# Kernel optimization log

Hardware: AMD Instinct MI355X
Metric: run time of the kernel (lower is better)

## Reference

```python
import jax, jax.numpy as jnp
import numpy as np

B, N, S = 8, 4096, 1024
D1, D2 = 128, 256
IN_CH, OUT_CH = D1 + D2, 256
BN_EPS = 1e-5


def setup_inputs() -> dict:
    key = jax.random.key(0)
    ks = jax.random.split(key, 12)
    inp = {
        "xyz1": jax.random.normal(ks[0], (B, N, 3), jnp.float32),
        "xyz2": jax.random.normal(ks[1], (B, S, 3), jnp.float32),
        "points1": jax.random.normal(ks[2], (B, N, D1), jnp.float32),
        "points2": jax.random.normal(ks[3], (B, S, D2), jnp.float32),
        # fuse: Conv1d(in_ch->out_ch, k=1) + BN
        "W_fuse": jax.random.normal(ks[4], (OUT_CH, IN_CH), jnp.float32) * (1.0 / np.sqrt(IN_CH)),
        "b_fuse": jnp.zeros((OUT_CH,), jnp.float32),
        "g_fuse": jnp.ones((OUT_CH,), jnp.float32),
        "bt_fuse": jnp.zeros((OUT_CH,), jnp.float32),
        # res block net1: Conv1d(out_ch->out_ch) + BN (res_expansion=1.0)
        "W1": jax.random.normal(ks[5], (OUT_CH, OUT_CH), jnp.float32) * (1.0 / np.sqrt(OUT_CH)),
        "b1": jnp.zeros((OUT_CH,), jnp.float32),
        "g1": jnp.ones((OUT_CH,), jnp.float32),
        "bt1": jnp.zeros((OUT_CH,), jnp.float32),
        # res block net2: Conv1d(out_ch->out_ch) + BN
        "W2": jax.random.normal(ks[6], (OUT_CH, OUT_CH), jnp.float32) * (1.0 / np.sqrt(OUT_CH)),
        "b2": jnp.zeros((OUT_CH,), jnp.float32),
        "g2": jnp.ones((OUT_CH,), jnp.float32),
        "bt2": jnp.zeros((OUT_CH,), jnp.float32),
    }
    return inp


def _bn(x, g, b):
    # BatchNorm1d training-mode forward: stats over (batch, length), x: [B, C, L]
    m = jnp.mean(x, axis=(0, 2), keepdims=True)
    v = jnp.var(x, axis=(0, 2), keepdims=True)
    return (x - m) * jax.lax.rsqrt(v + BN_EPS) * g[None, :, None] + b[None, :, None]


def _conv1x1(x, W, b):
    # x: [B, C_in, L], W: [C_out, C_in] -> [B, C_out, L]
    return jnp.einsum("oc,bcl->bol", W, x) + b[None, :, None]


def _gelu(x):
    return jax.nn.gelu(x, approximate=False)  # torch nn.GELU default (erf)


def reference(xyz1, xyz2, points1, points2,
              W_fuse, b_fuse, g_fuse, bt_fuse,
              W1, b1, g1, bt1, W2, b2, g2, bt2):
    # squared pairwise distances [B, N, S] without B x N x S x 3 intermediate
    d = (jnp.sum(xyz1 * xyz1, -1)[:, :, None]
         - 2.0 * jnp.einsum("bnc,bsc->bns", xyz1, xyz2)
         + jnp.sum(xyz2 * xyz2, -1)[:, None, :])
    # 3 nearest coarse points per dense point (== sort ascending, take first 3)
    neg_d3, idx = jax.lax.top_k(-d, 3)            # [B, N, 3]
    d3 = -neg_d3
    recip = 1.0 / (d3 + 1e-8)
    w = recip / jnp.sum(recip, axis=2, keepdims=True)  # [B, N, 3]
    gathered = points2[jnp.arange(points2.shape[0])[:, None, None], idx]  # [B, N, 3, D2]
    interp = jnp.sum(gathered * w[..., None], axis=2)  # [B, N, D2]

    new_points = jnp.concatenate([points1, interp], axis=-1)  # [B, N, D1+D2]
    x = jnp.transpose(new_points, (0, 2, 1))                   # [B, C, N]

    # fuse: conv-bn-gelu
    x = _gelu(_bn(_conv1x1(x, W_fuse, b_fuse), g_fuse, bt_fuse))
    # residual block: gelu(bn(conv(gelu(bn(conv(x))))) + x)
    y = _gelu(_bn(_conv1x1(x, W1, b1), g1, bt1))
    y = _bn(_conv1x1(y, W2, b2), g2, bt2)
    x = _gelu(y + x)

    return jnp.transpose(x, (0, 2, 1))  # [B, N, out_ch]
```

## Files before the change

### kernel.cpp

```cpp
#include <hip/hip_runtime.h>
#include <hip/hip_bf16.h>

constexpr int Bb = 8, Nn = 4096, Ss = 1024;
constexpr int D1 = 128, D2 = 256, KIN = 384, OC = 256;
constexpr int L = Bb * Nn;
constexpr float BN_EPS = 1e-5f;

typedef __attribute__((ext_vector_type(4))) float floatx4;
typedef __attribute__((ext_vector_type(8))) __bf16 bf16x8;

#define DEV __device__ __forceinline__

DEV float bf2f(unsigned short u) {
    union { unsigned int i; float f; } v; v.i = ((unsigned int)u) << 16; return v.f;
}
DEV unsigned short f2bf(float f) {
    union { float f; unsigned int i; } v; v.f = f;
    unsigned int x = v.i;
    return (unsigned short)((x + 0x7FFFu + ((x >> 16) & 1u)) >> 16);
}
DEV float gelu_f(float x) {
    float u = x * (0.7978845608f + 0.0356774081f * x * x);
    float t = __expf(-2.0f * u);
    return x * __builtin_amdgcn_rcpf(1.0f + t);
}

DEV bool probe_isf(const unsigned int* __restrict__ w, int tid) {
    unsigned int lo = w[tid & 63] & 0xFFFFu;
    int e = (int)((lo >> 7) & 0xFF);
    unsigned long long m = __ballot(e >= 100 && e <= 144);
    return __popcll(m) < 48;
}

template <int K> DEV int permoff(int off) {
    int row = off / K, rr = off - row * K;
    int cg_ = (rr >> 3) & 7;
    return row * K + (rr & ~63) + (((cg_ ^ (row & 7)) << 3)) + (rr & 7);
}

DEV void merge3(float& d0, float& d1, float& d2, int& i0, int& i1, int& i2,
                float e0, float e1, float e2, int j0, int j1, int j2, bool pref) {
    float a0 = d0, a1 = d1, a2 = d2; int x0 = i0, x1 = i1, x2 = i2;
    float b0 = e0, b1 = e1;          int y0 = j0, y1 = j1;
    bool t = pref ? (a0 <= b0) : (a0 < b0);
    d0 = t ? a0 : b0; i0 = t ? x0 : y0;
    a0 = t ? a1 : a0; x0 = t ? x1 : x0;
    a1 = t ? a2 : a1; x1 = t ? x2 : x1;
    b0 = t ? b0 : b1; y0 = t ? y0 : y1;
    b1 = t ? b1 : e2; y1 = t ? y1 : j2;
    t = pref ? (a0 <= b0) : (a0 < b0);
    d1 = t ? a0 : b0; i1 = t ? x0 : y0;
    a0 = t ? a1 : a0; x0 = t ? x1 : x0;
    b0 = t ? b0 : b1; y0 = t ? y0 : y1;
    t = pref ? (a0 <= b0) : (a0 < b0);
    d2 = t ? a0 : b0; i2 = t ? x0 : y0;
}

__global__ __launch_bounds__(256) void k_front(const void* __restrict__ xyz1_,
                                               const void* __restrict__ xyz2_,
                                               const void* __restrict__ w0_,
                                               const void* __restrict__ w1_,
                                               const void* __restrict__ w2_,
                                               unsigned short* __restrict__ Wdst,
                                               float* __restrict__ stats,
                                               int* __restrict__ dflag,
                                               int* __restrict__ nn_idx,
                                               float* __restrict__ nn_w) {
    int tid = threadIdx.x;
    int bid = blockIdx.x;
    bool isf = probe_isf((const unsigned int*)xyz1_, tid);

    if (bid < 6) {
        stats[bid * 256 + tid] = 0.0f;
        if (bid == 0 && tid == 0) *dflag = isf ? 1 : 0;
        return;
    }
    if (bid < 902) {
        int i = (bid - 6) * 256 + tid;
        const void* src; int off;
        if (i < 98304)       { src = w0_; off = permoff<384>(i); }
        else if (i < 163840) { src = w1_; off = permoff<256>(i - 98304); }
        else                 { src = w2_; off = permoff<256>(i - 163840); }
        Wdst[i] = isf ? f2bf(((const float*)src)[off]) : ((const unsigned short*)src)[off];
        return;
    }

    __shared__ alignas(16) float s4[Ss * 4 + 32];
    int bn0 = (bid - 902) * 32;
    int b = bn0 >> 12;

    if (isf) {
        const float* p2 = (const float*)xyz2_ + (size_t)b * Ss * 3;
        for (int i = tid; i < Ss * 3; i += 256) {
            int s = i / 3, k = i - s * 3;
            s4[s * 4 + k + ((s >> 7) << 2)] = p2[i];
        }
    } else {
        const unsigned short* p2 = (const unsigned short*)xyz2_ + (size_t)b * Ss * 3;
        for (int i = tid; i < Ss * 3; i += 256) {
            int s = i / 3, k = i - s * 3;
            s4[s * 4 + k + ((s >> 7) << 2)] = bf2f(p2[i]);
        }
    }
    __syncthreads();
    for (int s = tid; s < Ss; s += 256) {
        int a = s * 4 + ((s >> 7) << 2);
        float x = s4[a], y = s4[a + 1], z = s4[a + 2];
        s4[a + 3] = x * x + y * y + z * z;
    }
    __syncthreads();

    int part = tid & 7;
    int bn = bn0 + (tid >> 3);
    float x1, y1, z1;
    if (isf) {
        const float* p1 = (const float*)xyz1_ + (size_t)bn * 3;
        x1 = p1[0]; y1 = p1[1]; z1 = p1[2];
    } else {
        const unsigned short* p1 = (const unsigned short*)xyz1_ + (size_t)bn * 3;
        x1 = bf2f(p1[0]); y1 = bf2f(p1[1]); z1 = bf2f(p1[2]);
    }
    float n1 = x1 * x1 + y1 * y1 + z1 * z1;

    float d0 = 3.4e38f, d1 = 3.4e38f, d2 = 3.4e38f;
    int i0 = 0, i1 = 0, i2 = 0;
    const float* sp = &s4[part * 516];
#pragma unroll 4
    for (int j = 0; j < 128; ++j) {
        float4 qv = *(const float4*)(sp + j * 4);
        float d = n1 + qv.w - 2.0f * (x1 * qv.x + y1 * qv.y + z1 * qv.z);
        int s = part * 128 + j;
        bool c2 = d < d2, c1 = d < d1, c0 = d < d0;
        d2 = c1 ? d1 : (c2 ? d : d2); i2 = c1 ? i1 : (c2 ? s : i2);
        d1 = c0 ? d0 : (c1 ? d : d1); i1 = c0 ? i0 : (c1 ? s : i1);
        d0 = c0 ? d  : d0;            i0 = c0 ? s  : i0;
    }
#pragma unroll
    for (int m = 1; m <= 4; m <<= 1) {
        float e0 = __shfl_xor(d0, m, 64), e1 = __shfl_xor(d1, m, 64), e2 = __shfl_xor(d2, m, 64);
        int   j0 = __shfl_xor(i0, m, 64), j1 = __shfl_xor(i1, m, 64), j2 = __shfl_xor(i2, m, 64);
        bool pref = (part < (part ^ m));
        merge3(d0, d1, d2, i0, i1, i2, e0, e1, e2, j0, j1, j2, pref);
    }
    if (part == 0) {
        float r0 = 1.0f / (d0 + 1e-8f), r1 = 1.0f / (d1 + 1e-8f), r2 = 1.0f / (d2 + 1e-8f);
        float rs = 1.0f / (r0 + r1 + r2);
        nn_idx[bn * 3 + 0] = i0; nn_idx[bn * 3 + 1] = i1; nn_idx[bn * 3 + 2] = i2;
        nn_w[bn * 3 + 0] = r0 * rs; nn_w[bn * 3 + 1] = r1 * rs; nn_w[bn * 3 + 2] = r2 * rs;
    }
}

__global__ __launch_bounds__(256, 4) void k_gemm1(const void* __restrict__ p1_,
                                                  const void* __restrict__ p2_,
                                                  const int* __restrict__ nn_idx,
                                                  const float* __restrict__ nn_w,
                                                  const int* __restrict__ dflag,
                                                  const unsigned short* __restrict__ W,
                                                  unsigned short* __restrict__ Out,
                                                  float* __restrict__ S1, float* __restrict__ S2) {
    __shared__ alignas(16) unsigned short As[32 * 64];
    __shared__ alignas(16) unsigned short Bs[256 * 64];
    __shared__ float sS1[256], sS2[256];

    int tid = threadIdx.x;
    int l0 = blockIdx.x * 32;
    int wn = tid >> 6, lane = tid & 63, quad = lane >> 4, lr = lane & 15;
    bool isf = (*dflag != 0);

    floatx4 acc[2][4];
#pragma unroll
    for (int mi = 0; mi < 2; ++mi)
#pragma unroll
        for (int ni = 0; ni < 4; ++ni) acc[mi][ni] = (floatx4){0.f, 0.f, 0.f, 0.f};

    for (int kc = 0; kc < KIN / 64; ++kc) {
        __syncthreads();
#pragma unroll
        for (int it = 0; it < 8; ++it) {
            int chunk = it * 4 + wn;
            int row = chunk * 8 + (lane >> 3);
            int cg_ = lane & 7;
            const unsigned short* src = W + (size_t)row * KIN + kc * 64 + cg_ * 8;
            __builtin_amdgcn_global_load_lds(
                (const __attribute__((address_space(1))) void*)src,
                (__attribute__((address_space(3))) void*)&Bs[chunk * 512],
                16, 0, 0);
        }
        {
            int row = tid >> 3, c8 = tid & 7;
            int pt = l0 + row;
            int c0 = kc * 64 + c8 * 8;
            union { uint4 v; unsigned short u[8]; } va;
            if (c0 < D1) {
                if (isf) {
                    const float* p = (const float*)p1_ + (size_t)pt * D1 + c0;
                    float4 f0 = *(const float4*)p;
                    float4 f1 = *(const float4*)(p + 4);
                    va.u[0] = f2bf(f0.x); va.u[1] = f2bf(f0.y); va.u[2] = f2bf(f0.z); va.u[3] = f2bf(f0.w);
                    va.u[4] = f2bf(f1.x); va.u[5] = f2bf(f1.y); va.u[6] = f2bf(f1.z); va.u[7] = f2bf(f1.w);
                } else {
                    va.v = *(const uint4*)((const unsigned short*)p1_ + (size_t)pt * D1 + c0);
                }
            } else {
                int c2 = c0 - D1;
                int b = pt >> 12;
                int j0 = nn_idx[pt * 3], j1 = nn_idx[pt * 3 + 1], j2 = nn_idx[pt * 3 + 2];
                float w0 = nn_w[pt * 3], w1 = nn_w[pt * 3 + 1], w2 = nn_w[pt * 3 + 2];
                if (isf) {
                    const float* base = (const float*)p2_;
                    const float* r0 = base + ((size_t)(b * Ss + j0)) * D2 + c2;
                    const float* r1 = base + ((size_t)(b * Ss + j1)) * D2 + c2;
                    const float* r2 = base + ((size_t)(b * Ss + j2)) * D2 + c2;
#pragma unroll
                    for (int h = 0; h < 2; ++h) {
                        float4 a0 = *(const float4*)(r0 + h * 4);
                        float4 a1 = *(const float4*)(r1 + h * 4);
                        float4 a2 = *(const float4*)(r2 + h * 4);
                        va.u[h * 4 + 0] = f2bf(w0 * a0.x + w1 * a1.x + w2 * a2.x);
                        va.u[h * 4 + 1] = f2bf(w0 * a0.y + w1 * a1.y + w2 * a2.y);
                        va.u[h * 4 + 2] = f2bf(w0 * a0.z + w1 * a1.z + w2 * a2.z);
                        va.u[h * 4 + 3] = f2bf(w0 * a0.w + w1 * a1.w + w2 * a2.w);
                    }
                } else {
                    const unsigned short* base = (const unsigned short*)p2_;
                    uint4 v0 = *(const uint4*)(base + ((size_t)(b * Ss + j0)) * D2 + c2);
                    uint4 v1 = *(const uint4*)(base + ((size_t)(b * Ss + j1)) * D2 + c2);
                    uint4 v2 = *(const uint4*)(base + ((size_t)(b * Ss + j2)) * D2 + c2);
                    const unsigned short* u0 = (const unsigned short*)&v0;
                    const unsigned short* u1 = (const unsigned short*)&v1;
                    const unsigned short* u2 = (const unsigned short*)&v2;
#pragma unroll
                    for (int j = 0; j < 8; ++j)
                        va.u[j] = f2bf(w0 * bf2f(u0[j]) + w1 * bf2f(u1[j]) + w2 * bf2f(u2[j]));
                }
            }
            *(uint4*)&As[row * 64 + ((c8 ^ (row & 7)) << 3)] = va.v;
        }
        __syncthreads();
#pragma unroll
        for (int ks8 = 0; ks8 < 2; ++ks8) {
            bf16x8 af[2], bfr[4];
#pragma unroll
            for (int mi = 0; mi < 2; ++mi) {
                int ra = mi * 16 + lr;
                af[mi] = *(const bf16x8*)&As[ra * 64 + ((((ks8 << 2) + quad) ^ (ra & 7)) << 3)];
            }
#pragma unroll
            for (int ni = 0; ni < 4; ++ni) {
                int rb = wn * 64 + ni * 16 + lr;
                bfr[ni] = *(const bf16x8*)&Bs[rb * 64 + ((((ks8 << 2) + quad) ^ (rb & 7)) << 3)];
            }
#pragma unroll
            for (int mi = 0; mi < 2; ++mi)
#pragma unroll
                for (int ni = 0; ni < 4; ++ni)
                    acc[mi][ni] = __builtin_amdgcn_mfma_f32_16x16x32_bf16(af[mi], bfr[ni], acc[mi][ni], 0, 0, 0);
        }
    }

    float p1a[4] = {0, 0, 0, 0}, p2a[4] = {0, 0, 0, 0};
#pragma unroll
    for (int mi = 0; mi < 2; ++mi)
#pragma unroll
        for (int ni = 0; ni < 4; ++ni)
#pragma unroll
            for (int r = 0; r < 4; ++r) {
                float v = acc[mi][ni][r];
                int row = l0 + mi * 16 + quad * 4 + r;
                int col = wn * 64 + ni * 16 + lr;
                Out[(size_t)row * OC + col] = f2bf(v);
                p1a[ni] += v; p2a[ni] += v * v;
            }
    sS1[tid] = 0.f; sS2[tid] = 0.f;
    __syncthreads();
#pragma unroll
    for (int ni = 0; ni < 4; ++ni) {
        atomicAdd(&sS1[wn * 64 + ni * 16 + lr], p1a[ni]);
        atomicAdd(&sS2[wn * 64 + ni * 16 + lr], p2a[ni]);
    }
    __syncthreads();
    atomicAdd(&S1[tid], sS1[tid]);
    atomicAdd(&S2[tid], sS2[tid]);
}

__global__ __launch_bounds__(256, 4) void k_gemm(const unsigned short* __restrict__ A,
                                                 const unsigned short* __restrict__ W,
                                                 unsigned short* __restrict__ Out,
                                                 float* __restrict__ S1, float* __restrict__ S2,
                                                 const float* __restrict__ S1in,
                                                 const float* __restrict__ S2in,
                                                 const void* __restrict__ g_,
                                                 const void* __restrict__ bt_,
                                                 const int* __restrict__ dflag) {
    __shared__ alignas(16) unsigned short As[64 * 64];
    __shared__ alignas(16) unsigned short Bs[128 * 64];
    __shared__ float sS1[128], sS2[128];
    __shared__ float sCA[256], sCC[256];

    int tid = threadIdx.x;
    int l0 = (blockIdx.x >> 1) * 64;
    int n0 = (blockIdx.x & 1) * 128;
    int wn = tid >> 6, lane = tid & 63, quad = lane >> 4, lr = lane & 15;
    int wr = wn >> 1, wc = wn & 1;

    {
        float m = S1in[tid] * (1.0f / (float)L);
        float var = S2in[tid] * (1.0f / (float)L) - m * m;
        float g, bt;
        if (*dflag) { g = ((const float*)g_)[tid]; bt = ((const float*)bt_)[tid]; }
        else { g = bf2f(((const unsigned short*)g_)[tid]); bt = bf2f(((const unsigned short*)bt_)[tid]); }
        float a = g * rsqrtf(var + BN_EPS);
        sCA[tid] = a;
        sCC[tid] = bt - m * a;
        if (tid < 128) { sS1[tid] = 0.f; sS2[tid] = 0.f; }
    }

    floatx4 acc[2][4];
#pragma unroll
    for (int mi = 0; mi < 2; ++mi)
#pragma unroll
        for (int ni = 0; ni < 4; ++ni) acc[mi][ni] = (floatx4){0.f, 0.f, 0.f, 0.f};

    for (int kc = 0; kc < OC / 64; ++kc) {
        __syncthreads();
#pragma unroll
        for (int it = 0; it < 4; ++it) {
            int chunk = it * 4 + wn;
            int row = chunk * 8 + (lane >> 3);
            int cg_ = lane & 7;
            const unsigned short* src = W + (size_t)(n0 + row) * OC + kc * 64 + cg_ * 8;
            __builtin_amdgcn_global_load_lds(
                (const __attribute__((address_space(1))) void*)src,
                (__attribute__((address_space(3))) void*)&Bs[chunk * 512],
                16, 0, 0);
        }
#pragma unroll
        for (int it = 0; it < 2; ++it) {
            int idx = it * 256 + tid, row = idx >> 3, c8 = idx & 7;
            union { uint4 v; unsigned short u[8]; } va;
            va.v = *(const uint4*)(A + (size_t)(l0 + row) * OC + kc * 64 + c8 * 8);
            int kb = kc * 64 + c8 * 8;
#pragma unroll
            for (int j = 0; j < 8; ++j) {
                float f = bf2f(va.u[j]);
                va.u[j] = f2bf(gelu_f(sCA[kb + j] * f + sCC[kb + j]));
            }
            *(uint4*)&As[row * 64 + ((c8 ^ (row & 7)) << 3)] = va.v;
        }
        __syncthreads();
#pragma unroll
        for (int ks8 = 0; ks8 < 2; ++ks8) {
            bf16x8 af[2], bfr[4];
#pragma unroll
            for (int mi = 0; mi < 2; ++mi) {
                int ra = wr * 32 + mi * 16 + lr;
                af[mi] = *(const bf16x8*)&As[ra * 64 + ((((ks8 << 2) + quad) ^ (ra & 7)) << 3)];
            }
#pragma unroll
            for (int ni = 0; ni < 4; ++ni) {
                int rb = wc * 64 + ni * 16 + lr;
                bfr[ni] = *(const bf16x8*)&Bs[rb * 64 + ((((ks8 << 2) + quad) ^ (rb & 7)) << 3)];
            }
#pragma unroll
            for (int mi = 0; mi < 2; ++mi)
#pragma unroll
                for (int ni = 0; ni < 4; ++ni)
                    acc[mi][ni] = __builtin_amdgcn_mfma_f32_16x16x32_bf16(af[mi], bfr[ni], acc[mi][ni], 0, 0, 0);
        }
    }

    float p1a[4] = {0, 0, 0, 0}, p2a[4] = {0, 0, 0, 0};
#pragma unroll
    for (int mi = 0; mi < 2; ++mi)
#pragma unroll
        for (int ni = 0; ni < 4; ++ni)
#pragma unroll
            for (int r = 0; r < 4; ++r) {
                float v = acc[mi][ni][r];
                int row = l0 + wr * 32 + mi * 16 + quad * 4 + r;
                int col = n0 + wc * 64 + ni * 16 + lr;
                Out[(size_t)row * OC + col] = f2bf(v);
                p1a[ni] += v; p2a[ni] += v * v;
            }
    __syncthreads();
#pragma unroll
    for (int ni = 0; ni < 4; ++ni) {
        atomicAdd(&sS1[wc * 64 + ni * 16 + lr], p1a[ni]);
        atomicAdd(&sS2[wc * 64 + ni * 16 + lr], p2a[ni]);
    }
    __syncthreads();
    if (tid < 128) {
        atomicAdd(&S1[n0 + tid], sS1[tid]);
        atomicAdd(&S2[n0 + tid], sS2[tid]);
    }
}

__global__ __launch_bounds__(256) void k_final(const unsigned short* __restrict__ t0,
                                               const unsigned short* __restrict__ t2,
                                               const float* __restrict__ S1_0, const float* __restrict__ S2_0,
                                               const float* __restrict__ S1_2, const float* __restrict__ S2_2,
                                               const void* __restrict__ g0_, const void* __restrict__ bt0_,
                                               const void* __restrict__ g2_, const void* __restrict__ bt2_,
                                               const int* __restrict__ dflag,
                                               void* __restrict__ out_) {
    __shared__ float sA0[256], sC0[256], sA2[256], sC2[256];
    int tid = threadIdx.x;
    bool isf = (*dflag != 0);
    {
        float m0 = S1_0[tid] * (1.0f / (float)L);
        float v0_ = S2_0[tid] * (1.0f / (float)L) - m0 * m0;
        float m2 = S1_2[tid] * (1.0f / (float)L);
        float v2_ = S2_2[tid] * (1.0f / (float)L) - m2 * m2;
        float g0, b0, g2, b2;
        if (isf) {
            g0 = ((const float*)g0_)[tid]; b0 = ((const float*)bt0_)[tid];
            g2 = ((const float*)g2_)[tid]; b2 = ((const float*)bt2_)[tid];
        } else {
            g0 = bf2f(((const unsigned short*)g0_)[tid]); b0 = bf2f(((const unsigned short*)bt0_)[tid]);
            g2 = bf2f(((const unsigned short*)g2_)[tid]); b2 = bf2f(((const unsigned short*)bt2_)[tid]);
        }
        float a0 = g0 * rsqrtf(v0_ + BN_EPS);
        float a2 = g2 * rsqrtf(v2_ + BN_EPS);
        sA0[tid] = a0; sC0[tid] = b0 - m0 * a0;
        sA2[tid] = a2; sC2[tid] = b2 - m2 * a2;
    }
    __syncthreads();

    int idx = (blockIdx.x * 256 + tid) * 8;
    int col = idx & (OC - 1);
    union { uint4 v; unsigned short u[8]; } v0, v2;
    v0.v = *(const uint4*)(t0 + idx);
    v2.v = *(const uint4*)(t2 + idx);
    float r[8];
#pragma unroll
    for (int j = 0; j < 8; ++j) {
        float x = gelu_f(sA0[col + j] * bf2f(v0.u[j]) + sC0[col + j]);
        float y = sA2[col + j] * bf2f(v2.u[j]) + sC2[col + j];
        r[j] = gelu_f(x + y);
    }
    if (isf) {
        float* o = (float*)out_ + idx;
        float4 lo = {r[0], r[1], r[2], r[3]};
        float4 hi = {r[4], r[5], r[6], r[7]};
        *(float4*)o = lo;
        *(float4*)(o + 4) = hi;
    } else {
        union { uint4 v; unsigned short u[8]; } vo;
#pragma unroll
        for (int j = 0; j < 8; ++j) vo.u[j] = f2bf(r[j]);
        *(uint4*)((unsigned short*)out_ + idx) = vo.v;
    }
}

extern "C" void kernel_launch(void* const* d_in, const int* in_sizes, int n_in,
                              void* d_out, int out_size, void* d_ws, size_t ws_size,
                              hipStream_t stream) {
    const void* xyz1    = d_in[0];
    const void* xyz2    = d_in[1];
    const void* points1 = d_in[2];
    const void* points2 = d_in[3];
    const void* W_fuse  = d_in[4];
    const void* g_fuse  = d_in[6];
    const void* bt_fuse = d_in[7];
    const void* W1      = d_in[8];
    const void* g1      = d_in[10];
    const void* bt1     = d_in[11];
    const void* W2      = d_in[12];
    const void* g2      = d_in[14];
    const void* bt2     = d_in[15];

    char* ws = (char*)d_ws;
    unsigned short* t2 = (unsigned short*)ws;
    unsigned short* t0 = (unsigned short*)(ws + 25165824);
    unsigned short* t1 = (unsigned short*)d_out;
    int*   nn_idx = (int*)(ws + 41943040);
    float* nn_w   = (float*)(ws + 42336256);
    float* stats  = (float*)(ws + 42729472);
    int*   dflag  = (int*)(ws + 42729472 + 3072 * 4);
    unsigned short* Wbf = (unsigned short*)(ws + 42745856);

    float *S1_0 = stats,        *S2_0 = stats + 256;
    float *S1_1 = stats + 512,  *S2_1 = stats + 768;
    float *S1_2 = stats + 1024, *S2_2 = stats + 1280;

    k_front<<<1926, 256, 0, stream>>>(xyz1, xyz2, W_fuse, W1, W2, Wbf, stats, dflag, nn_idx, nn_w);
    k_gemm1<<<L / 32, 256, 0, stream>>>(points1, points2, nn_idx, nn_w, dflag,
                                        Wbf, t0, S1_0, S2_0);
    k_gemm<<<(L / 64) * 2, 256, 0, stream>>>(t0, Wbf + 98304, t1, S1_1, S2_1,
                                             S1_0, S2_0, g_fuse, bt_fuse, dflag);
    k_gemm<<<(L / 64) * 2, 256, 0, stream>>>(t1, Wbf + 163840, t2, S1_2, S2_2,
                                             S1_1, S2_1, g1, bt1, dflag);
    k_final<<<L * OC / (256 * 8), 256, 0, stream>>>(t0, t2, S1_0, S2_0, S1_2, S2_2,
                                                    g_fuse, bt_fuse, g2, bt2, dflag, d_out);
}
```

Before: 235.6 us.

## Split interpolation into separate kernel and shrink GEMM tiles to 32x128

The interpolation and concat that were fused into the first GEMM's A-tile load now run in a separate k_interp kernel. It writes a pre-swizzled bf16 X matrix into the output buffer. The first GEMM then becomes a template instance that streams A straight into LDS with global_load_lds. All GEMMs now use 32-row by 128-column tiles with 2048 blocks, which raises parallelism and cuts per-thread accumulators. The cost is an extra kernel launch and a full write and read of the 32768x384 bf16 intermediate, and the smaller tiles reuse less data per block.

```diff
diff --git a/kernel.cpp b/kernel.cpp
--- a/kernel.cpp
+++ b/kernel.cpp
@@ -150,139 +150,70 @@
     }
 }
 
-__global__ __launch_bounds__(256, 4) void k_gemm1(const void* __restrict__ p1_,
-                                                  const void* __restrict__ p2_,
-                                                  const int* __restrict__ nn_idx,
-                                                  const float* __restrict__ nn_w,
-                                                  const int* __restrict__ dflag,
-                                                  const unsigned short* __restrict__ W,
-                                                  unsigned short* __restrict__ Out,
-                                                  float* __restrict__ S1, float* __restrict__ S2) {
-    __shared__ alignas(16) unsigned short As[32 * 64];
-    __shared__ alignas(16) unsigned short Bs[256 * 64];
-    __shared__ float sS1[256], sS2[256];
-
-    int tid = threadIdx.x;
-    int l0 = blockIdx.x * 32;
-    int wn = tid >> 6, lane = tid & 63, quad = lane >> 4, lr = lane & 15;
+__global__ __launch_bounds__(256) void k_interp(const void* __restrict__ p1_,
+                                                const void* __restrict__ p2_,
+                                                const int* __restrict__ nn_idx,
+                                                const float* __restrict__ nn_w,
+                                                const int* __restrict__ dflag,
+                                                unsigned short* __restrict__ X) {
     bool isf = (*dflag != 0);
-
-    floatx4 acc[2][4];
-#pragma unroll
-    for (int mi = 0; mi < 2; ++mi)
-#pragma unroll
-        for (int ni = 0; ni < 4; ++ni) acc[mi][ni] = (floatx4){0.f, 0.f, 0.f, 0.f};
-
-    for (int kc = 0; kc < KIN / 64; ++kc) {
-        __syncthreads();
-#pragma unroll
-        for (int it = 0; it < 8; ++it) {
-            int chunk = it * 4 + wn;
-            int row = chunk * 8 + (lane >> 3);
-            int cg_ = lane & 7;
-            const unsigned short* src = W + (size_t)row * KIN + kc * 64 + cg_ * 8;
-            __builtin_amdgcn_global_load_lds(
-                (const __attribute__((address_space(1))) void*)src,
-                (__attribute__((address_space(3))) void*)&Bs[chunk * 512],
-                16, 0, 0);
-        }
-        {
-            int row = tid >> 3, c8 = tid & 7;
-            int pt = l0 + row;
-            int c0 = kc * 64 + c8 * 8;
-            union { uint4 v; unsigned short u[8]; } va;
-            if (c0 < D1) {
-                if (isf) {
-                    const float* p = (const float*)p1_ + (size_t)pt * D1 + c0;
-                    float4 f0 = *(const float4*)p;
-                    float4 f1 = *(const float4*)(p + 4);
-                    va.u[0] = f2bf(f0.x); va.u[1] = f2bf(f0.y); va.u[2] = f2bf(f0.z); va.u[3] = f2bf(f0.w);
-                    va.u[4] = f2bf(f1.x); va.u[5] = f2bf(f1.y); va.u[6] = f2bf(f1.z); va.u[7] = f2bf(f1.w);
-                } else {
-                    va.v = *(const uint4*)((const unsigned short*)p1_ + (size_t)pt * D1 + c0);
+    int i0_ = blockIdx.x * 256 + threadIdx.x;
+    constexpr int GPR = KIN / 8;
+#pragma unroll
+    for (int it = 0; it < 3; ++it) {
+        int g = i0_ + it * 524288;
+        int row = g / GPR, cg = g - row * GPR;
+        int chunk = cg >> 3, cgc = cg & 7;
+        union { uint4 v; unsigned short u[8]; } va;
+        if (cg < 16) {
+            int c0 = cg * 8;
+            if (isf) {
+                const float* p = (const float*)p1_ + (size_t)row * D1 + c0;
+                float4 f0 = *(const float4*)p;
+                float4 f1 = *(const float4*)(p + 4);
+                va.u[0] = f2bf(f0.x); va.u[1] = f2bf(f0.y); va.u[2] = f2bf(f0.z); va.u[3] = f2bf(f0.w);
+                va.u[4] = f2bf(f1.x); va.u[5] = f2bf(f1.y); va.u[6] = f2bf(f1.z); va.u[7] = f2bf(f1.w);
+            } else {
+                va.v = *(const uint4*)((const unsigned short*)p1_ + (size_t)row * D1 + c0);
+            }
+        } else {
+            int c2 = (cg - 16) * 8;
+            int b = row >> 12;
+            int j0 = nn_idx[row * 3], j1 = nn_idx[row * 3 + 1], j2 = nn_idx[row * 3 + 2];
+            float w0 = nn_w[row * 3], w1 = nn_w[row * 3 + 1], w2 = nn_w[row * 3 + 2];
+            if (isf) {
+                const float* base = (const float*)p2_;
+                const float* r0 = base + ((size_t)(b * Ss + j0)) * D2 + c2;
+                const float* r1 = base + ((size_t)(b * Ss + j1)) * D2 + c2;
+                const float* r2 = base + ((size_t)(b * Ss + j2)) * D2 + c2;
+#pragma unroll
+                for (int h = 0; h < 2; ++h) {
+                    float4 a0 = *(const float4*)(r0 + h * 4);
+                    float4 a1 = *(const float4*)(r1 + h * 4);
+                    float4 a2 = *(const float4*)(r2 + h * 4);
+                    va.u[h * 4 + 0] = f2bf(w0 * a0.x + w1 * a1.x + w2 * a2.x);
+                    va.u[h * 4 + 1] = f2bf(w0 * a0.y + w1 * a1.y + w2 * a2.y);
+                    va.u[h * 4 + 2] = f2bf(w0 * a0.z + w1 * a1.z + w2 * a2.z);
+                    va.u[h * 4 + 3] = f2bf(w0 * a0.w + w1 * a1.w + w2 * a2.w);
                 }
             } else {
-                int c2 = c0 - D1;
-                int b = pt >> 12;
-                int j0 = nn_idx[pt * 3], j1 = nn_idx[pt * 3 + 1], j2 = nn_idx[pt * 3 + 2];
-                float w0 = nn_w[pt * 3], w1 = nn_w[pt * 3 + 1], w2 = nn_w[pt * 3 + 2];
-                if (isf) {
-                    const float* base = (const float*)p2_;
-                    const float* r0 = base + ((size_t)(b * Ss + j0)) * D2 + c2;
-                    const float* r1 = base + ((size_t)(b * Ss + j1)) * D2 + c2;
-                    const float* r2 = base + ((size_t)(b * Ss + j2)) * D2 + c2;
-#pragma unroll
-                    for (int h = 0; h < 2; ++h) {
-                        float4 a0 = *(const float4*)(r0 + h * 4);
-                        float4 a1 = *(const float4*)(r1 + h * 4);
-                        float4 a2 = *(const float4*)(r2 + h * 4);
-                        va.u[h * 4 + 0] = f2bf(w0 * a0.x + w1 * a1.x + w2 * a2.x);
-                        va.u[h * 4 + 1] = f2bf(w0 * a0.y + w1 * a1.y + w2 * a2.y);
-                        va.u[h * 4 + 2] = f2bf(w0 * a0.z + w1 * a1.z + w2 * a2.z);
-                        va.u[h * 4 + 3] = f2bf(w0 * a0.w + w1 * a1.w + w2 * a2.w);
-                    }
-                } else {
-                    const unsigned short* base = (const unsigned short*)p2_;
-                    uint4 v0 = *(const uint4*)(base + ((size_t)(b * Ss + j0)) * D2 + c2);
-                    uint4 v1 = *(const uint4*)(base + ((size_t)(b * Ss + j1)) * D2 + c2);
-                    uint4 v2 = *(const uint4*)(base + ((size_t)(b * Ss + j2)) * D2 + c2);
-                    const unsigned short* u0 = (const unsigned short*)&v0;
-                    const unsigned short* u1 = (const unsigned short*)&v1;
-                    const unsigned short* u2 = (const unsigned short*)&v2;
-#pragma unroll
-                    for (int j = 0; j < 8; ++j)
-                        va.u[j] = f2bf(w0 * bf2f(u0[j]) + w1 * bf2f(u1[j]) + w2 * bf2f(u2[j]));
-                }
-            }
-            *(uint4*)&As[row * 64 + ((c8 ^ (row & 7)) << 3)] = va.v;
-        }
-        __syncthreads();
-#pragma unroll
-        for (int ks8 = 0; ks8 < 2; ++ks8) {
-            bf16x8 af[2], bfr[4];
-#pragma unroll
-            for (int mi = 0; mi < 2; ++mi) {
-                int ra = mi * 16 + lr;
-                af[mi] = *(const bf16x8*)&As[ra * 64 + ((((ks8 << 2) + quad) ^ (ra & 7)) << 3)];
-            }
-#pragma unroll
-            for (int ni = 0; ni < 4; ++ni) {
-                int rb = wn * 64 + ni * 16 + lr;
-                bfr[ni] = *(const bf16x8*)&Bs[rb * 64 + ((((ks8 << 2) + quad) ^ (rb & 7)) << 3)];
-            }
-#pragma unroll
-            for (int mi = 0; mi < 2; ++mi)
-#pragma unroll
-                for (int ni = 0; ni < 4; ++ni)
-                    acc[mi][ni] = __builtin_amdgcn_mfma_f32_16x16x32_bf16(af[mi], bfr[ni], acc[mi][ni], 0, 0, 0);
-        }
-    }
-
-    float p1a[4] = {0, 0, 0, 0}, p2a[4] = {0, 0, 0, 0};
-#pragma unroll
-    for (int mi = 0; mi < 2; ++mi)
-#pragma unroll
-        for (int ni = 0; ni < 4; ++ni)
-#pragma unroll
-            for (int r = 0; r < 4; ++r) {
-                float v = acc[mi][ni][r];
-                int row = l0 + mi * 16 + quad * 4 + r;
-                int col = wn * 64 + ni * 16 + lr;
-                Out[(size_t)row * OC + col] = f2bf(v);
-                p1a[ni] += v; p2a[ni] += v * v;
-            }
-    sS1[tid] = 0.f; sS2[tid] = 0.f;
-    __syncthreads();
-#pragma unroll
-    for (int ni = 0; ni < 4; ++ni) {
-        atomicAdd(&sS1[wn * 64 + ni * 16 + lr], p1a[ni]);
-        atomicAdd(&sS2[wn * 64 + ni * 16 + lr], p2a[ni]);
-    }
-    __syncthreads();
-    atomicAdd(&S1[tid], sS1[tid]);
-    atomicAdd(&S2[tid], sS2[tid]);
-}
-
+                const unsigned short* base = (const unsigned short*)p2_;
+                uint4 v0 = *(const uint4*)(base + ((size_t)(b * Ss + j0)) * D2 + c2);
+                uint4 v1 = *(const uint4*)(base + ((size_t)(b * Ss + j1)) * D2 + c2);
+                uint4 v2 = *(const uint4*)(base + ((size_t)(b * Ss + j2)) * D2 + c2);
+                const unsigned short* u0 = (const unsigned short*)&v0;
+                const unsigned short* u1 = (const unsigned short*)&v1;
+                const unsigned short* u2 = (const unsigned short*)&v2;
+#pragma unroll
+                for (int j = 0; j < 8; ++j)
+                    va.u[j] = f2bf(w0 * bf2f(u0[j]) + w1 * bf2f(u1[j]) + w2 * bf2f(u2[j]));
+            }
+        }
+        *(uint4*)&X[(size_t)row * KIN + chunk * 64 + ((cgc ^ (row & 7)) << 3)] = va.v;
+    }
+}
+
+template <int K, bool ACT>
 __global__ __launch_bounds__(256, 4) void k_gemm(const unsigned short* __restrict__ A,
                                                  const unsigned short* __restrict__ W,
                                                  unsigned short* __restrict__ Out,
@@ -292,18 +223,17 @@
                                                  const void* __restrict__ g_,
                                                  const void* __restrict__ bt_,
                                                  const int* __restrict__ dflag) {
-    __shared__ alignas(16) unsigned short As[64 * 64];
+    __shared__ alignas(16) unsigned short As[32 * 64];
     __shared__ alignas(16) unsigned short Bs[128 * 64];
     __shared__ float sS1[128], sS2[128];
     __shared__ float sCA[256], sCC[256];
 
     int tid = threadIdx.x;
-    int l0 = (blockIdx.x >> 1) * 64;
+    int l0 = (blockIdx.x >> 1) * 32;
     int n0 = (blockIdx.x & 1) * 128;
     int wn = tid >> 6, lane = tid & 63, quad = lane >> 4, lr = lane & 15;
-    int wr = wn >> 1, wc = wn & 1;
-
-    {
+
+    if constexpr (ACT) {
         float m = S1in[tid] * (1.0f / (float)L);
         float var = S2in[tid] * (1.0f / (float)L) - m * m;
         float g, bt;
@@ -312,33 +242,37 @@
         float a = g * rsqrtf(var + BN_EPS);
         sCA[tid] = a;
         sCC[tid] = bt - m * a;
-        if (tid < 128) { sS1[tid] = 0.f; sS2[tid] = 0.f; }
-    }
-
-    floatx4 acc[2][4];
+    }
+    if (tid < 128) { sS1[tid] = 0.f; sS2[tid] = 0.f; }
+
+    floatx4 acc[2][2];
 #pragma unroll
     for (int mi = 0; mi < 2; ++mi)
 #pragma unroll
-        for (int ni = 0; ni < 4; ++ni) acc[mi][ni] = (floatx4){0.f, 0.f, 0.f, 0.f};
-
-    for (int kc = 0; kc < OC / 64; ++kc) {
+        for (int ni = 0; ni < 2; ++ni) acc[mi][ni] = (floatx4){0.f, 0.f, 0.f, 0.f};
+
+    for (int kc = 0; kc < K / 64; ++kc) {
         __syncthreads();
 #pragma unroll
         for (int it = 0; it < 4; ++it) {
             int chunk = it * 4 + wn;
             int row = chunk * 8 + (lane >> 3);
-            int cg_ = lane & 7;
-            const unsigned short* src = W + (size_t)(n0 + row) * OC + kc * 64 + cg_ * 8;
+            const unsigned short* src = W + (size_t)(n0 + row) * K + kc * 64 + (lane & 7) * 8;
             __builtin_amdgcn_global_load_lds(
                 (const __attribute__((address_space(1))) void*)src,
                 (__attribute__((address_space(3))) void*)&Bs[chunk * 512],
                 16, 0, 0);
         }
-#pragma unroll
-        for (int it = 0; it < 2; ++it) {
-            int idx = it * 256 + tid, row = idx >> 3, c8 = idx & 7;
+        if constexpr (!ACT) {
+            const unsigned short* src = A + (size_t)(l0 + wn * 8 + (lane >> 3)) * K + kc * 64 + (lane & 7) * 8;
+            __builtin_amdgcn_global_load_lds(
+                (const __attribute__((address_space(1))) void*)src,
+                (__attribute__((address_space(3))) void*)&As[wn * 512],
+                16, 0, 0);
+        } else {
+            int row = tid >> 3, c8 = tid & 7;
             union { uint4 v; unsigned short u[8]; } va;
-            va.v = *(const uint4*)(A + (size_t)(l0 + row) * OC + kc * 64 + c8 * 8);
+            va.v = *(const uint4*)(A + (size_t)(l0 + row) * K + kc * 64 + c8 * 8);
             int kb = kc * 64 + c8 * 8;
 #pragma unroll
             for (int j = 0; j < 8; ++j) {
@@ -350,43 +284,43 @@
         __syncthreads();
 #pragma unroll
         for (int ks8 = 0; ks8 < 2; ++ks8) {
-            bf16x8 af[2], bfr[4];
+            bf16x8 af[2], bfr[2];
 #pragma unroll
             for (int mi = 0; mi < 2; ++mi) {
-                int ra = wr * 32 + mi * 16 + lr;
+                int ra = mi * 16 + lr;
                 af[mi] = *(const bf16x8*)&As[ra * 64 + ((((ks8 << 2) + quad) ^ (ra & 7)) << 3)];
             }
 #pragma unroll
-            for (int ni = 0; ni < 4; ++ni) {
-                int rb = wc * 64 + ni * 16 + lr;
+            for (int ni = 0; ni < 2; ++ni) {
+                int rb = wn * 32 + ni * 16 + lr;
                 bfr[ni] = *(const bf16x8*)&Bs[rb * 64 + ((((ks8 << 2) + quad) ^ (rb & 7)) << 3)];
             }
 #pragma unroll
             for (int mi = 0; mi < 2; ++mi)
 #pragma unroll
-                for (int ni = 0; ni < 4; ++ni)
+                for (int ni = 0; ni < 2; ++ni)
                     acc[mi][ni] = __builtin_amdgcn_mfma_f32_16x16x32_bf16(af[mi], bfr[ni], acc[mi][ni], 0, 0, 0);
         }
     }
 
-    float p1a[4] = {0, 0, 0, 0}, p2a[4] = {0, 0, 0, 0};
+    float p1a[2] = {0, 0}, p2a[2] = {0, 0};
 #pragma unroll
     for (int mi = 0; mi < 2; ++mi)
 #pragma unroll
-        for (int ni = 0; ni < 4; ++ni)
+        for (int ni = 0; ni < 2; ++ni)
 #pragma unroll
             for (int r = 0; r < 4; ++r) {
                 float v = acc[mi][ni][r];
-                int row = l0 + wr * 32 + mi * 16 + quad * 4 + r;
-                int col = n0 + wc * 64 + ni * 16 + lr;
+                int row = l0 + mi * 16 + quad * 4 + r;
+                int col = n0 + wn * 32 + ni * 16 + lr;
                 Out[(size_t)row * OC + col] = f2bf(v);
                 p1a[ni] += v; p2a[ni] += v * v;
             }
     __syncthreads();
 #pragma unroll
-    for (int ni = 0; ni < 4; ++ni) {
-        atomicAdd(&sS1[wc * 64 + ni * 16 + lr], p1a[ni]);
-        atomicAdd(&sS2[wc * 64 + ni * 16 + lr], p2a[ni]);
+    for (int ni = 0; ni < 2; ++ni) {
+        atomicAdd(&sS1[wn * 32 + ni * 16 + lr], p1a[ni]);
+        atomicAdd(&sS2[wn * 32 + ni * 16 + lr], p2a[ni]);
     }
     __syncthreads();
     if (tid < 128) {
@@ -472,6 +406,7 @@
     char* ws = (char*)d_ws;
     unsigned short* t2 = (unsigned short*)ws;
     unsigned short* t0 = (unsigned short*)(ws + 25165824);
+    unsigned short* X  = (unsigned short*)d_out;
     unsigned short* t1 = (unsigned short*)d_out;
     int*   nn_idx = (int*)(ws + 41943040);
     float* nn_w   = (float*)(ws + 42336256);
@@ -484,12 +419,13 @@
     float *S1_2 = stats + 1024, *S2_2 = stats + 1280;
 
     k_front<<<1926, 256, 0, stream>>>(xyz1, xyz2, W_fuse, W1, W2, Wbf, stats, dflag, nn_idx, nn_w);
-    k_gemm1<<<L / 32, 256, 0, stream>>>(points1, points2, nn_idx, nn_w, dflag,
-                                        Wbf, t0, S1_0, S2_0);
-    k_gemm<<<(L / 64) * 2, 256, 0, stream>>>(t0, Wbf + 98304, t1, S1_1, S2_1,
-                                             S1_0, S2_0, g_fuse, bt_fuse, dflag);
-    k_gemm<<<(L / 64) * 2, 256, 0, stream>>>(t1, Wbf + 163840, t2, S1_2, S2_2,
-                                             S1_1, S2_1, g1, bt1, dflag);
+    k_interp<<<2048, 256, 0, stream>>>(points1, points2, nn_idx, nn_w, dflag, X);
+    k_gemm<KIN, false><<<2048, 256, 0, stream>>>(X, Wbf, t0, S1_0, S2_0,
+                                                 nullptr, nullptr, nullptr, nullptr, dflag);
+    k_gemm<OC, true><<<2048, 256, 0, stream>>>(t0, Wbf + 98304, t1, S1_1, S2_1,
+                                               S1_0, S2_0, g_fuse, bt_fuse, dflag);
+    k_gemm<OC, true><<<2048, 256, 0, stream>>>(t1, Wbf + 163840, t2, S1_2, S2_2,
+                                               S1_1, S2_1, g1, bt1, dflag);
     k_final<<<L * OC / (256 * 8), 256, 0, stream>>>(t0, t2, S1_0, S2_0, S1_2, S2_2,
                                                     g_fuse, bt_fuse, g2, bt2, dflag, d_out);
 }
```

New measurement: 272.1 us. 1.15x slower.
